# Optimization experiments

Measured on AMD Instinct MI355X. Metric: run time of the kernel, lower is better.

Reference implementation:

```python
import jax, jax.numpy as jnp
import numpy as np
import math

D_MODEL = 768
N_HEADS = 6
HD = D_MODEL // N_HEADS  # 128
RANK = D_MODEL // 4      # 192
B, T = 128, 256


def _rope_tables(T, dim):
    # matches torch: inv = 1/10000**(arange(0,dim,2)/dim); emb = cat([outer(t,inv)]*2, -1)
    inv = 1.0 / (10000.0 ** (jnp.arange(0, dim, 2, dtype=jnp.float32) / dim))
    t = jnp.arange(T, dtype=jnp.float32)
    freqs = jnp.outer(t, inv)                       # [T, dim/2]
    emb = jnp.concatenate([freqs, freqs], axis=-1)  # [T, dim]
    return jnp.cos(emb), jnp.sin(emb)               # each [T, dim]


def _rot(x):
    h = x.shape[-1] // 2
    return jnp.concatenate([-x[..., h:], x[..., :h]], axis=-1)


def setup_inputs() -> dict:
    key = jax.random.key(0)
    ks = jax.random.split(key, 8)
    s_in = 1.0 / math.sqrt(D_MODEL)
    s_r = 1.0 / math.sqrt(RANK)
    inp = {
        'x': jax.random.normal(ks[0], (B, T, D_MODEL), dtype=jnp.float32),
        'qA': jax.random.normal(ks[1], (D_MODEL, RANK), dtype=jnp.float32) * s_in,
        'qB': jax.random.normal(ks[2], (RANK, D_MODEL), dtype=jnp.float32) * s_r,
        'kA': jax.random.normal(ks[3], (D_MODEL, RANK), dtype=jnp.float32) * s_in,
        'kB': jax.random.normal(ks[4], (RANK, D_MODEL), dtype=jnp.float32) * s_r,
        'vA': jax.random.normal(ks[5], (D_MODEL, RANK), dtype=jnp.float32) * s_in,
        'vB': jax.random.normal(ks[6], (RANK, D_MODEL), dtype=jnp.float32) * s_r,
        'o_w': jax.random.normal(ks[7], (D_MODEL, D_MODEL), dtype=jnp.float32) * s_in,
    }
    return inp


def reference(x, qA, qB, kA, kB, vA, vB, o_w):
    Bb, Tt, _ = x.shape
    # low-rank projections: in -> rank -> out, then split heads [B, H, T, hd]
    def proj(A, W):
        h = (x @ A) @ W
        return h.reshape(Bb, Tt, N_HEADS, HD).transpose(0, 2, 1, 3)
    q = proj(qA, qB)
    k = proj(kA, kB)
    v = proj(vA, vB)
    cos, sin = _rope_tables(Tt, HD)  # [T, hd], broadcast over B, H
    q = q * cos + _rot(q) * sin
    k = k * cos + _rot(k) * sin
    att = jnp.einsum('bhqd,bhkd->bhqk', q, k) / math.sqrt(HD)
    causal = jnp.tril(jnp.ones((Tt, Tt), dtype=bool))
    att = jnp.where(causal, att, -jnp.inf)
    att = jax.nn.softmax(att, axis=-1)
    out = jnp.einsum('bhqk,bhkd->bhqd', att, v)          # [B, H, T, hd]
    out = out.transpose(0, 2, 1, 3).reshape(Bb, Tt, D_MODEL)
    return out @ o_w
```

## Files before the change

kernel.cpp:

```cpp
#include <hip/hip_runtime.h>
#include <hip/hip_bf16.h>
#include <stdint.h>

typedef __attribute__((ext_vector_type(8))) short s16x8;
typedef __attribute__((ext_vector_type(4))) float f32x4;

#define D_MODEL 768
#define N_HEADS 6
#define HD 128
#define RANK 192
#define TT 256
#define NROW 32768
#define NK 12
#define QSCL 0.08838834764831845f
#define PSTRIDE 25165824

__device__ inline short f2bf(float f) {
  union { float f; unsigned u; } x; x.f = f;
  unsigned r = x.u + 0x7fffu + ((x.u >> 16) & 1u);
  return (short)(r >> 16);
}
__device__ inline float bf2f(short v) {
  union { unsigned u; float f; } x; x.u = ((unsigned)(unsigned short)v) << 16;
  return x.f;
}
__device__ inline void gload_lds16(const void* g, void* lds) {
  __builtin_amdgcn_global_load_lds(
      (const __attribute__((address_space(1))) unsigned int*)g,
      (__attribute__((address_space(3))) unsigned int*)lds, 16, 0, 0);
}

#define BAR()    asm volatile("s_barrier" ::: "memory")
#define LGKM0()  asm volatile("s_waitcnt lgkmcnt(0)" ::: "memory")
#define WAITVM4() asm volatile("s_waitcnt vmcnt(4)" ::: "memory")
#define WAITVM0() asm volatile("s_waitcnt vmcnt(0)" ::: "memory")

__global__ void k_tables(float* __restrict__ cosT, float* __restrict__ sinT) {
  int tid = blockIdx.x * 256 + threadIdx.x;
  int t = tid >> 6, i = tid & 63;
  float inv = powf(10000.0f, -(float)i / 64.0f);
  float ang = (float)t * inv;
  cosT[tid] = cosf(ang);
  sinT[tid] = sinf(ang);
}

__global__ void k_castx(const float* __restrict__ x, short* __restrict__ xb) {
  int t = blockIdx.x * 256 + threadIdx.x;
  const float4* xp = (const float4*)x;
  float4 a = xp[t * 2], b = xp[t * 2 + 1];
  s16x8 o;
  o[0] = f2bf(a.x); o[1] = f2bf(a.y); o[2] = f2bf(a.z); o[3] = f2bf(a.w);
  o[4] = f2bf(b.x); o[5] = f2bf(b.y); o[6] = f2bf(b.z); o[7] = f2bf(b.w);
  *(s16x8*)(xb + (size_t)t * 8) = o;
}

__global__ void k_makew(const float* __restrict__ qA, const float* __restrict__ qB,
                        const float* __restrict__ kA, const float* __restrict__ kB,
                        const float* __restrict__ vA, const float* __restrict__ vB,
                        short* __restrict__ WT) {
  int g = blockIdx.x * 256 + threadIdx.x;
  int n4 = g % 576, kkb = g / 576;
  int part = n4 / 192, nnb = (n4 % 192) * 4;
  const float* A = (part == 0) ? qA : (part == 1) ? kA : vA;
  const float* Bm = (part == 0) ? qB : (part == 1) ? kB : vB;
  float acc[4][4] = {};
  for (int r0 = 0; r0 < RANK; r0 += 4) {
    float4 a4[4], b4[4];
#pragma unroll
    for (int q = 0; q < 4; ++q)
      a4[q] = *(const float4*)&A[(kkb + q * 192) * RANK + r0];
#pragma unroll
    for (int i = 0; i < 4; ++i)
      b4[i] = *(const float4*)&Bm[(r0 + i) * 768 + nnb];
#pragma unroll
    for (int q = 0; q < 4; ++q) {
      const float* aq = (const float*)&a4[q];
#pragma unroll
      for (int i = 0; i < 4; ++i) {
        const float* bi = (const float*)&b4[i];
#pragma unroll
        for (int jn = 0; jn < 4; ++jn)
          acc[q][jn] += aq[i] * bi[jn];
      }
    }
  }
#pragma unroll
  for (int q = 0; q < 4; ++q)
#pragma unroll
    for (int jn = 0; jn < 4; ++jn)
      WT[(size_t)(part * 768 + nnb + jn) * 768 + kkb + q * 192] = f2bf(acc[q][jn]);
}

__global__ void k_wot(const float* __restrict__ ow, short* __restrict__ WT) {
  int g = blockIdx.x * 256 + threadIdx.x;
  int n = g % 768, kk = g / 768;
  WT[(size_t)(2304 + n) * 768 + kk] = f2bf(ow[(size_t)kk * 768 + n]);
}

__device__ inline s16x8 rdfrag(const short* hbase, int rowbyte, int ksl4x, int swz) {
  return *(const s16x8*)((const char*)hbase + rowbyte + (((ksl4x) ^ (swz)) << 4));
}

template <int MODE>
__global__ __launch_bounds__(512, 2) void k_gemm8(const short* __restrict__ A,
                                                  const short* __restrict__ Bt,
                                                  void* __restrict__ Cv, int ldc) {
  extern __shared__ short lds[];
  const int tid = threadIdx.x;
  const int wid = tid >> 6, lane = tid & 63;
  const int l15 = lane & 15, l4 = lane >> 4;
  const int wr = wid >> 2, wc = wid & 3;
  const int swz = l15 & 7;
  const int bid = blockIdx.y * 128 + blockIdx.x;
  const int nper = gridDim.y;
  const int xcd = bid & 7, loc = bid >> 3;
  const int mq = loc / nper;
  const int mt = xcd * 16 + mq;
  const int nt = loc - mq * nper;
  const long mbase = (long)mt * 256;
  const long nbase = (long)nt * 256;

  const int hb0 = wid * 2048 + lane * 16;
  const int hb1 = hb0 + 1024;
  const int r0 = hb0 >> 7, c0 = ((hb0 >> 4) & 7) ^ (r0 & 7);
  const int r1 = hb1 >> 7, c1 = ((hb1 >> 4) & 7) ^ (r1 & 7);
  const int off0 = r0 * 768 + c0 * 8;
  const int off1 = r1 * 768 + c1 * 8;

#define STAGE(G, rowoff, kt, ldsS) do {                                        \
    gload_lds16((G) + (size_t)(rowoff) * 768 + (kt) * 64 + off0,               \
                (char*)(ldsS) + wid * 2048);                                   \
    gload_lds16((G) + (size_t)(rowoff) * 768 + (kt) * 64 + off1,               \
                (char*)(ldsS) + wid * 2048 + 1024);                            \
  } while (0)

#define LDSA(buf, half) (lds + ((buf) * 2 + (half)) * 8192)
#define LDSB(buf, half) (lds + 32768 + ((buf) * 2 + (half)) * 8192)

  f32x4 acc[8][4] = {};

  STAGE(A,  mbase,       0, LDSA(0, 0));
  STAGE(Bt, nbase,       0, LDSB(0, 0));
  STAGE(A,  mbase + 128, 0, LDSA(0, 1));
  STAGE(Bt, nbase + 128, 0, LDSB(0, 1));
  STAGE(A,  mbase,       1, LDSA(1, 0));
  STAGE(Bt, nbase,       1, LDSB(1, 0));
  WAITVM4();
  BAR();

  s16x8 a03[4][2], a47[4][2], b01[2][2], b23[2][2];

#pragma unroll
  for (int kt = 0; kt < NK; ++kt) {
    const int buf = kt & 1, nbuf = buf ^ 1;
    const short* Ab = LDSA(buf, wr);
    const short* Bb = LDSB(buf, (wc >> 1));
    const int browbase = (wc & 1) * 64 * 128;

#pragma unroll
    for (int mf = 0; mf < 4; ++mf)
#pragma unroll
      for (int ks = 0; ks < 2; ++ks)
        a03[mf][ks] = rdfrag(Ab, (mf * 16 + l15) * 128, ks * 4 + l4, swz);
#pragma unroll
    for (int nf = 0; nf < 2; ++nf)
#pragma unroll
      for (int ks = 0; ks < 2; ++ks)
        b01[nf][ks] = rdfrag(Bb, browbase + (nf * 16 + l15) * 128, ks * 4 + l4, swz);
    if (kt + 1 < NK) STAGE(A, mbase + 128, kt + 1, LDSA(nbuf, 1));
    BAR();
    LGKM0();
    __builtin_amdgcn_s_setprio(1);
#pragma unroll
    for (int mf = 0; mf < 4; ++mf)
#pragma unroll
      for (int nf = 0; nf < 2; ++nf)
#pragma unroll
        for (int ks = 0; ks < 2; ++ks)
          acc[mf][nf] = __builtin_amdgcn_mfma_f32_16x16x32_bf16(a03[mf][ks], b01[nf][ks], acc[mf][nf], 0, 0, 0);
    __builtin_amdgcn_s_setprio(0);
    BAR();

#pragma unroll
    for (int mf = 0; mf < 4; ++mf)
#pragma unroll
      for (int ks = 0; ks < 2; ++ks)
        a47[mf][ks] = rdfrag(Ab, ((mf + 4) * 16 + l15) * 128, ks * 4 + l4, swz);
    if (kt + 1 < NK) STAGE(Bt, nbase + 128, kt + 1, LDSB(nbuf, 1));
    BAR();
    LGKM0();
    __builtin_amdgcn_s_setprio(1);
#pragma unroll
    for (int mf = 0; mf < 4; ++mf)
#pragma unroll
      for (int nf = 0; nf < 2; ++nf)
#pragma unroll
        for (int ks = 0; ks < 2; ++ks)
          acc[mf + 4][nf] = __builtin_amdgcn_mfma_f32_16x16x32_bf16(a47[mf][ks], b01[nf][ks], acc[mf + 4][nf], 0, 0, 0);
    __builtin_amdgcn_s_setprio(0);
    BAR();

#pragma unroll
    for (int nf = 0; nf < 2; ++nf)
#pragma unroll
      for (int ks = 0; ks < 2; ++ks)
        b23[nf][ks] = rdfrag(Bb, browbase + ((nf + 2) * 16 + l15) * 128, ks * 4 + l4, swz);
    if (kt + 2 < NK) STAGE(A, mbase, kt + 2, LDSA(buf, 0));
    BAR();
    LGKM0();
    __builtin_amdgcn_s_setprio(1);
#pragma unroll
    for (int mf = 0; mf < 4; ++mf)
#pragma unroll
      for (int nf = 0; nf < 2; ++nf)
#pragma unroll
        for (int ks = 0; ks < 2; ++ks)
          acc[mf][nf + 2] = __builtin_amdgcn_mfma_f32_16x16x32_bf16(a03[mf][ks], b23[nf][ks], acc[mf][nf + 2], 0, 0, 0);
    __builtin_amdgcn_s_setprio(0);
    BAR();

    if (kt + 2 < NK) STAGE(Bt, nbase, kt + 2, LDSB(buf, 0));
    BAR();
    __builtin_amdgcn_s_setprio(1);
#pragma unroll
    for (int mf = 0; mf < 4; ++mf)
#pragma unroll
      for (int nf = 0; nf < 2; ++nf)
#pragma unroll
        for (int ks = 0; ks < 2; ++ks)
          acc[mf + 4][nf + 2] = __builtin_amdgcn_mfma_f32_16x16x32_bf16(a47[mf][ks], b23[nf][ks], acc[mf + 4][nf + 2], 0, 0, 0);
    __builtin_amdgcn_s_setprio(0);
    if (kt < NK - 1) {
      if (kt + 2 < NK) WAITVM4(); else WAITVM0();
      BAR();
    }
  }
#undef STAGE

#pragma unroll
  for (int mf = 0; mf < 8; ++mf)
#pragma unroll
    for (int nf = 0; nf < 4; ++nf) {
      const int col = (int)(nbase + wc * 64 + nf * 16 + l15);
      const int part = col / 768;
      const int wi = col - part * 768;
      const int hh = wi >> 7, dd = wi & 127;
#pragma unroll
      for (int r = 0; r < 4; ++r) {
        long row = mbase + wr * 128 + mf * 16 + l4 * 4 + r;
        if (MODE == 0) {
          ((float*)Cv)[row * ldc + col] = acc[mf][nf][r];
        } else {
          size_t idx = (size_t)part * PSTRIDE +
                       (((size_t)(row >> 8) * 6 + hh) * 256 + (row & 255)) * 128 + dd;
          ((short*)Cv)[idx] = f2bf(acc[mf][nf][r]);
        }
      }
    }
}

__global__ void k_ropek(short* __restrict__ kp, const float* __restrict__ cosT,
                        const float* __restrict__ sinT) {
  int tid = blockIdx.x * 256 + threadIdx.x;
  int bh = tid >> 11, rem = tid & 2047;
  int t = rem >> 3, i8 = (rem & 7) * 8;
  size_t base = ((size_t)bh * 256 + t) * 128 + i8;
  s16x8 a = *(const s16x8*)(kp + base);
  s16x8 b = *(const s16x8*)(kp + base + 64);
  const float4* cp = (const float4*)(cosT + t * 64 + i8);
  const float4* sp = (const float4*)(sinT + t * 64 + i8);
  float4 c04 = cp[0], c14 = cp[1], s04 = sp[0], s14 = sp[1];
  float cs[8] = {c04.x, c04.y, c04.z, c04.w, c14.x, c14.y, c14.z, c14.w};
  float sn[8] = {s04.x, s04.y, s04.z, s04.w, s14.x, s14.y, s14.z, s14.w};
  s16x8 na, nb;
#pragma unroll
  for (int j = 0; j < 8; ++j) {
    float av = bf2f(a[j]), bv = bf2f(b[j]);
    na[j] = f2bf(av * cs[j] - bv * sn[j]);
    nb[j] = f2bf(bv * cs[j] + av * sn[j]);
  }
  *(s16x8*)(kp + base) = na;
  *(s16x8*)(kp + base + 64) = nb;
}

__global__ __launch_bounds__(512) void k_attn(const short* __restrict__ qp,
                                              const short* __restrict__ kp,
                                              const short* __restrict__ vp,
                                              short* __restrict__ attout,
                                              const float* __restrict__ cosT,
                                              const float* __restrict__ sinT) {
  extern __shared__ short smem[];
  short* Kls0 = smem;
  short* Kls1 = smem + 8192;
  short* Vt   = smem + 16384;
  const int tid = threadIdx.x;
  const int wid = tid >> 6, lane = tid & 63;
  const int l15 = lane & 15, l4 = lane >> 4;
  short* PlsW = smem + 24576 + wid * 2048;
  const int bh = blockIdx.x;
  const int b = bh / N_HEADS, h = bh % N_HEADS;
  const long row0 = (long)b * TT;
  const size_t pbase = (size_t)bh * 256 * 128;
  const int d0 = wid * 16;

  s16x8 qf[2][4];
#pragma unroll
  for (int mi = 0; mi < 2; ++mi)
#pragma unroll
    for (int kc = 0; kc < 4; ++kc) {
      int t = wid * 32 + mi * 16 + l15;
      qf[mi][kc] = *(const s16x8*)(qp + pbase + (size_t)t * 128 + kc * 32 + l4 * 8);
    }
#pragma unroll
  for (int mi = 0; mi < 2; ++mi) {
    int t = wid * 32 + mi * 16 + l15;
#pragma unroll
    for (int kc = 0; kc < 2; ++kc) {
      const float4* cp = (const float4*)(cosT + t * 64 + kc * 32 + l4 * 8);
      const float4* sp = (const float4*)(sinT + t * 64 + kc * 32 + l4 * 8);
      float4 c04 = cp[0], c14 = cp[1], s04 = sp[0], s14 = sp[1];
      float cs[8] = {c04.x, c04.y, c04.z, c04.w, c14.x, c14.y, c14.z, c14.w};
      float sn[8] = {s04.x, s04.y, s04.z, s04.w, s14.x, s14.y, s14.z, s14.w};
#pragma unroll
      for (int jj = 0; jj < 8; ++jj) {
        float av = bf2f(qf[mi][kc][jj]);
        float bv = bf2f(qf[mi][kc + 2][jj]);
        qf[mi][kc][jj]     = f2bf((av * cs[jj] - bv * sn[jj]) * QSCL);
        qf[mi][kc + 2][jj] = f2bf((bv * cs[jj] + av * sn[jj]) * QSCL);
      }
    }
  }

#define STAGEK(j_, Kd) do {                                                     \
    int bb0_ = wid * 2048 + lane * 16;                                          \
    int r0_ = bb0_ >> 8; int sc0_ = ((bb0_ >> 4) & 15) ^ (r0_ & 7);             \
    gload_lds16(kp + pbase + (size_t)((j_) * 64 + r0_) * 128 + sc0_ * 8,        \
                (char*)(Kd) + wid * 2048);                                      \
    int bb1_ = bb0_ + 1024;                                                     \
    int r1_ = bb1_ >> 8; int sc1_ = ((bb1_ >> 4) & 15) ^ (r1_ & 7);             \
    gload_lds16(kp + pbase + (size_t)((j_) * 64 + r1_) * 128 + sc1_ * 8,        \
                (char*)(Kd) + wid * 2048 + 1024);                               \
  } while (0)

#define LOADV(j_, va, vb) do {                                                  \
    const short* vsrc_ = vp + pbase + (size_t)((j_) * 64 + lane) * 128 + d0;    \
    va = *(const s16x8*)vsrc_;                                                  \
    vb = *(const s16x8*)(vsrc_ + 8);                                            \
  } while (0)

  float mst[2][4], lst[2][4];
  f32x4 oacc[2][8];
#pragma unroll
  for (int mi = 0; mi < 2; ++mi)
#pragma unroll
    for (int r = 0; r < 4; ++r) { mst[mi][r] = -1e30f; lst[mi][r] = 0.f; }
#pragma unroll
  for (int mi = 0; mi < 2; ++mi)
#pragma unroll
    for (int nd = 0; nd < 8; ++nd) oacc[mi][nd] = {0.f, 0.f, 0.f, 0.f};

  const int jmax = (wid * 32 + 31) / 64;

  STAGEK(0, Kls0);
  s16x8 vr[2][2];
  LOADV(0, vr[0][0], vr[0][1]);

#pragma unroll
  for (int j = 0; j < 4; ++j) {
    const int buf = j & 1;
    const short* Kb = buf ? Kls1 : Kls0;
    short* Kn = buf ? Kls0 : Kls1;
    if (j < 3) {
      STAGEK(j + 1, Kn);
      LOADV(j + 1, vr[buf ^ 1][0], vr[buf ^ 1][1]);
    }
    if (j < 3) WAITVM4(); else WAITVM0();
    __builtin_amdgcn_sched_barrier(0);
    BAR();
#pragma unroll
    for (int e = 0; e < 8; ++e)
      *(short*)((char*)Vt + (d0 + e) * 128 + (((lane >> 3) ^ e) << 4) + (lane & 7) * 2) = vr[buf][0][e];
#pragma unroll
    for (int e = 0; e < 8; ++e)
      *(short*)((char*)Vt + (d0 + 8 + e) * 128 + (((lane >> 3) ^ e) << 4) + (lane & 7) * 2) = vr[buf][1][e];

    if (j <= jmax) {
      f32x4 sacc[2][4] = {};
#pragma unroll
      for (int kc = 0; kc < 4; ++kc) {
        s16x8 kf[4];
#pragma unroll
        for (int ni = 0; ni < 4; ++ni)
          kf[ni] = *(const s16x8*)((const char*)Kb + (ni * 16 + l15) * 256 +
                                   (((kc * 4 + l4) ^ (l15 & 7)) << 4));
#pragma unroll
        for (int mi = 0; mi < 2; ++mi)
#pragma unroll
          for (int ni = 0; ni < 4; ++ni)
            sacc[mi][ni] = __builtin_amdgcn_mfma_f32_16x16x32_bf16(qf[mi][kc], kf[ni], sacc[mi][ni], 0, 0, 0);
      }
#pragma unroll
      for (int mi = 0; mi < 2; ++mi) {
#pragma unroll
        for (int r = 0; r < 4; ++r) {
          int qr = wid * 32 + mi * 16 + l4 * 4 + r;
          float rm = -1e30f;
#pragma unroll
          for (int ni = 0; ni < 4; ++ni) {
            int kvc = j * 64 + ni * 16 + l15;
            if (kvc > qr) sacc[mi][ni][r] = -1e30f;
            rm = fmaxf(rm, sacc[mi][ni][r]);
          }
#pragma unroll
          for (int d2 = 1; d2 < 16; d2 <<= 1)
            rm = fmaxf(rm, __shfl_xor(rm, d2, 64));
          float mold = mst[mi][r];
          float mnew = fmaxf(mold, rm);
          float alpha = __expf(mold - mnew);
          mst[mi][r] = mnew;
          float rs = 0.f;
#pragma unroll
          for (int ni = 0; ni < 4; ++ni) {
            float p = __expf(sacc[mi][ni][r] - mnew);
            sacc[mi][ni][r] = p;
            rs += p;
          }
#pragma unroll
          for (int d2 = 1; d2 < 16; d2 <<= 1)
            rs += __shfl_xor(rs, d2, 64);
          lst[mi][r] = lst[mi][r] * alpha + rs;
#pragma unroll
          for (int nd = 0; nd < 8; ++nd)
            oacc[mi][nd][r] *= alpha;
        }
      }
#pragma unroll
      for (int mi = 0; mi < 2; ++mi)
#pragma unroll
        for (int ni = 0; ni < 4; ++ni)
#pragma unroll
          for (int r = 0; r < 4; ++r) {
            int prow = mi * 16 + l4 * 4 + r;
            int pcp = (ni * 2 + (l15 >> 3)) ^ (prow & 7);
            *(short*)((char*)PlsW + prow * 128 + (pcp << 4) + (l15 & 7) * 2) =
                f2bf(sacc[mi][ni][r]);
          }
    }
    LGKM0();
    BAR();
    __builtin_amdgcn_sched_barrier(0);
    if (j <= jmax) {
#pragma unroll
      for (int kc2 = 0; kc2 < 2; ++kc2) {
        s16x8 pa[2];
#pragma unroll
        for (int mi = 0; mi < 2; ++mi)
          pa[mi] = *(const s16x8*)((const char*)PlsW + (mi * 16 + l15) * 128 +
                                   (((kc2 * 4 + l4) ^ (l15 & 7)) << 4));
#pragma unroll
        for (int nd = 0; nd < 8; ++nd) {
          s16x8 vf = *(const s16x8*)((const char*)Vt + (nd * 16 + l15) * 128 +
                                     (((kc2 * 4 + l4) ^ (l15 & 7)) << 4));
#pragma unroll
          for (int mi = 0; mi < 2; ++mi)
            oacc[mi][nd] = __builtin_amdgcn_mfma_f32_16x16x32_bf16(pa[mi], vf, oacc[mi][nd], 0, 0, 0);
        }
      }
    }
  }
#undef STAGEK
#undef LOADV
#pragma unroll
  for (int mi = 0; mi < 2; ++mi)
#pragma unroll
    for (int nd = 0; nd < 8; ++nd)
#pragma unroll
      for (int r = 0; r < 4; ++r) {
        long row = row0 + wid * 32 + mi * 16 + l4 * 4 + r;
        int col = h * HD + nd * 16 + l15;
        attout[row * D_MODEL + col] = f2bf(oacc[mi][nd][r] / lst[mi][r]);
      }
}

extern "C" void kernel_launch(void* const* d_in, const int* in_sizes, int n_in,
                              void* d_out, int out_size, void* d_ws, size_t ws_size,
                              hipStream_t stream) {
  const float* x  = (const float*)d_in[0];
  const float* qA = (const float*)d_in[1];
  const float* qB = (const float*)d_in[2];
  const float* kA = (const float*)d_in[3];
  const float* kB = (const float*)d_in[4];
  const float* vA = (const float*)d_in[5];
  const float* vB = (const float*)d_in[6];
  const float* ow = (const float*)d_in[7];

  char* ws = (char*)d_ws;
  short* qkvp  = (short*)ws;
  short* qp    = qkvp;
  short* kp    = qkvp + (size_t)PSTRIDE;
  short* vp    = qkvp + (size_t)2 * PSTRIDE;
  short* xb    = (short*)(ws + 150994944);
  short* WT    = (short*)(ws + 201326592);
  float* cosT  = (float*)(ws + 206045184);
  float* sinT  = (float*)(ws + 206110720);
  short* attout = xb;

  hipFuncSetAttribute((const void*)k_gemm8<2>,
                      hipFuncAttributeMaxDynamicSharedMemorySize, 131072);
  hipFuncSetAttribute((const void*)k_gemm8<0>,
                      hipFuncAttributeMaxDynamicSharedMemorySize, 131072);
  hipFuncSetAttribute((const void*)k_attn,
                      hipFuncAttributeMaxDynamicSharedMemorySize, 81920);

  k_tables<<<64, 256, 0, stream>>>(cosT, sinT);
  k_castx<<<12288, 256, 0, stream>>>(x, xb);
  k_makew<<<432, 256, 0, stream>>>(qA, qB, kA, kB, vA, vB, WT);
  k_wot<<<2304, 256, 0, stream>>>(ow, WT);
  k_gemm8<2><<<dim3(128, 9), 512, 131072, stream>>>(xb, WT, (void*)qkvp, 0);
  k_ropek<<<6144, 256, 0, stream>>>(kp, cosT, sinT);
  k_attn<<<768, 512, 81920, stream>>>(qp, kp, vp, attout, cosT, sinT);
  k_gemm8<0><<<dim3(128, 3), 512, 131072, stream>>>(attout, WT + (size_t)2304 * 768, d_out, 768);
}
```

Before: 353.8 us.

## Compute QKV as two low-rank GEMMs instead of a prefused dense weight

Drops the kernel that multiplied A and B into a dense 768x2304 weight. Instead, x is multiplied by the concatenated A matrices (576 wide, padded to 768 tiles) into a bf16 intermediate h, and a second short-K GEMM applies the B matrices per part, writing head-split q, k and v. The GEMM kernel is templated on the K-tile count and on lda/ldb to support both stages. This roughly halves the projection FLOPs and removes the fp32 weight-fusion kernel, at the cost of an extra launch, writing and reading h, and padded columns in the first GEMM.

Result: slower. 365.6 us (+3.3%).

```diff
diff --git a/kernel.cpp b/kernel.cpp
--- a/kernel.cpp
+++ b/kernel.cpp
@@ -11,7 +11,6 @@
 #define RANK 192
 #define TT 256
 #define NROW 32768
-#define NK 12
 #define QSCL 0.08838834764831845f
 #define PSTRIDE 25165824
 
@@ -54,57 +53,39 @@
   *(s16x8*)(xb + (size_t)t * 8) = o;
 }
 
-__global__ void k_makew(const float* __restrict__ qA, const float* __restrict__ qB,
-                        const float* __restrict__ kA, const float* __restrict__ kB,
-                        const float* __restrict__ vA, const float* __restrict__ vB,
-                        short* __restrict__ WT) {
+__global__ void k_wt1(const float* __restrict__ qA, const float* __restrict__ kA,
+                      const float* __restrict__ vA, short* __restrict__ WT1) {
   int g = blockIdx.x * 256 + threadIdx.x;
-  int n4 = g % 576, kkb = g / 576;
-  int part = n4 / 192, nnb = (n4 % 192) * 4;
+  int n = g / 768, k = g % 768;
+  int part = n / RANK, r = n % RANK;
   const float* A = (part == 0) ? qA : (part == 1) ? kA : vA;
+  WT1[(size_t)n * 768 + k] = f2bf(A[(size_t)k * RANK + r]);
+}
+
+__global__ void k_wt2(const float* __restrict__ qB, const float* __restrict__ kB,
+                      const float* __restrict__ vB, short* __restrict__ WT2) {
+  int g = blockIdx.x * 256 + threadIdx.x;
+  int part = g / 147456, rem = g % 147456;
+  int r = rem / 768, n = rem % 768;
   const float* Bm = (part == 0) ? qB : (part == 1) ? kB : vB;
-  float acc[4][4] = {};
-  for (int r0 = 0; r0 < RANK; r0 += 4) {
-    float4 a4[4], b4[4];
-#pragma unroll
-    for (int q = 0; q < 4; ++q)
-      a4[q] = *(const float4*)&A[(kkb + q * 192) * RANK + r0];
-#pragma unroll
-    for (int i = 0; i < 4; ++i)
-      b4[i] = *(const float4*)&Bm[(r0 + i) * 768 + nnb];
-#pragma unroll
-    for (int q = 0; q < 4; ++q) {
-      const float* aq = (const float*)&a4[q];
-#pragma unroll
-      for (int i = 0; i < 4; ++i) {
-        const float* bi = (const float*)&b4[i];
-#pragma unroll
-        for (int jn = 0; jn < 4; ++jn)
-          acc[q][jn] += aq[i] * bi[jn];
-      }
-    }
-  }
-#pragma unroll
-  for (int q = 0; q < 4; ++q)
-#pragma unroll
-    for (int jn = 0; jn < 4; ++jn)
-      WT[(size_t)(part * 768 + nnb + jn) * 768 + kkb + q * 192] = f2bf(acc[q][jn]);
-}
-
-__global__ void k_wot(const float* __restrict__ ow, short* __restrict__ WT) {
+  WT2[(size_t)part * 147456 + (size_t)n * 192 + r] = f2bf(Bm[(size_t)r * 768 + n]);
+}
+
+__global__ void k_wot(const float* __restrict__ ow, short* __restrict__ WTo) {
   int g = blockIdx.x * 256 + threadIdx.x;
   int n = g % 768, kk = g / 768;
-  WT[(size_t)(2304 + n) * 768 + kk] = f2bf(ow[(size_t)kk * 768 + n]);
+  WTo[(size_t)n * 768 + kk] = f2bf(ow[(size_t)kk * 768 + n]);
 }
 
 __device__ inline s16x8 rdfrag(const short* hbase, int rowbyte, int ksl4x, int swz) {
   return *(const s16x8*)((const char*)hbase + rowbyte + (((ksl4x) ^ (swz)) << 4));
 }
 
-template <int MODE>
+template <int MODE, int NKT>
 __global__ __launch_bounds__(512, 2) void k_gemm8(const short* __restrict__ A,
                                                   const short* __restrict__ Bt,
-                                                  void* __restrict__ Cv, int ldc) {
+                                                  void* __restrict__ Cv,
+                                                  int lda, int ldb) {
   extern __shared__ short lds[];
   const int tid = threadIdx.x;
   const int wid = tid >> 6, lane = tid & 63;
@@ -117,41 +98,53 @@
   const int mq = loc / nper;
   const int mt = xcd * 16 + mq;
   const int nt = loc - mq * nper;
+  const int part  = (MODE == 2) ? (nt / 3) : 0;
+  const int ntile = (MODE == 2) ? (nt % 3) : nt;
   const long mbase = (long)mt * 256;
-  const long nbase = (long)nt * 256;
+  const long nbase = (long)ntile * 256;
+  const short* Aeff  = A + part * 192;
+  const short* Bteff = Bt + (size_t)part * 147456;
 
   const int hb0 = wid * 2048 + lane * 16;
   const int hb1 = hb0 + 1024;
   const int r0 = hb0 >> 7, c0 = ((hb0 >> 4) & 7) ^ (r0 & 7);
   const int r1 = hb1 >> 7, c1 = ((hb1 >> 4) & 7) ^ (r1 & 7);
-  const int off0 = r0 * 768 + c0 * 8;
-  const int off1 = r1 * 768 + c1 * 8;
-
-#define STAGE(G, rowoff, kt, ldsS) do {                                        \
-    gload_lds16((G) + (size_t)(rowoff) * 768 + (kt) * 64 + off0,               \
+  const int offA0 = r0 * lda + c0 * 8;
+  const int offA1 = r1 * lda + c1 * 8;
+  const int offB0 = r0 * ldb + c0 * 8;
+  const int offB1 = r1 * ldb + c1 * 8;
+
+#define STAGEA(rowbase, kt, ldsS) do {                                         \
+    gload_lds16(Aeff + (size_t)(rowbase) * lda + (kt) * 64 + offA0,            \
                 (char*)(ldsS) + wid * 2048);                                   \
-    gload_lds16((G) + (size_t)(rowoff) * 768 + (kt) * 64 + off1,               \
+    gload_lds16(Aeff + (size_t)(rowbase) * lda + (kt) * 64 + offA1,            \
                 (char*)(ldsS) + wid * 2048 + 1024);                            \
   } while (0)
+#define STAGEB(rowbase, kt, ldsS) do {                                         \
+    gload_lds16(Bteff + (size_t)(rowbase) * ldb + (kt) * 64 + offB0,           \
+                (char*)(ldsS) + wid * 2048);                                   \
+    gload_lds16(Bteff + (size_t)(rowbase) * ldb + (kt) * 64 + offB1,           \
+                (char*)(ldsS) + wid * 2048 + 1024);                            \
+  } while (0)
 
 #define LDSA(buf, half) (lds + ((buf) * 2 + (half)) * 8192)
 #define LDSB(buf, half) (lds + 32768 + ((buf) * 2 + (half)) * 8192)
 
   f32x4 acc[8][4] = {};
 
-  STAGE(A,  mbase,       0, LDSA(0, 0));
-  STAGE(Bt, nbase,       0, LDSB(0, 0));
-  STAGE(A,  mbase + 128, 0, LDSA(0, 1));
-  STAGE(Bt, nbase + 128, 0, LDSB(0, 1));
-  STAGE(A,  mbase,       1, LDSA(1, 0));
-  STAGE(Bt, nbase,       1, LDSB(1, 0));
+  STAGEA(mbase,       0, LDSA(0, 0));
+  STAGEB(nbase,       0, LDSB(0, 0));
+  STAGEA(mbase + 128, 0, LDSA(0, 1));
+  STAGEB(nbase + 128, 0, LDSB(0, 1));
+  STAGEA(mbase,       1, LDSA(1, 0));
+  STAGEB(nbase,       1, LDSB(1, 0));
   WAITVM4();
   BAR();
 
   s16x8 a03[4][2], a47[4][2], b01[2][2], b23[2][2];
 
 #pragma unroll
-  for (int kt = 0; kt < NK; ++kt) {
+  for (int kt = 0; kt < NKT; ++kt) {
     const int buf = kt & 1, nbuf = buf ^ 1;
     const short* Ab = LDSA(buf, wr);
     const short* Bb = LDSB(buf, (wc >> 1));
@@ -167,7 +160,7 @@
 #pragma unroll
       for (int ks = 0; ks < 2; ++ks)
         b01[nf][ks] = rdfrag(Bb, browbase + (nf * 16 + l15) * 128, ks * 4 + l4, swz);
-    if (kt + 1 < NK) STAGE(A, mbase + 128, kt + 1, LDSA(nbuf, 1));
+    if (kt + 1 < NKT) STAGEA(mbase + 128, kt + 1, LDSA(nbuf, 1));
     BAR();
     LGKM0();
     __builtin_amdgcn_s_setprio(1);
@@ -186,7 +179,7 @@
 #pragma unroll
       for (int ks = 0; ks < 2; ++ks)
         a47[mf][ks] = rdfrag(Ab, ((mf + 4) * 16 + l15) * 128, ks * 4 + l4, swz);
-    if (kt + 1 < NK) STAGE(Bt, nbase + 128, kt + 1, LDSB(nbuf, 1));
+    if (kt + 1 < NKT) STAGEB(nbase + 128, kt + 1, LDSB(nbuf, 1));
     BAR();
     LGKM0();
     __builtin_amdgcn_s_setprio(1);
@@ -205,7 +198,7 @@
 #pragma unroll
       for (int ks = 0; ks < 2; ++ks)
         b23[nf][ks] = rdfrag(Bb, browbase + ((nf + 2) * 16 + l15) * 128, ks * 4 + l4, swz);
-    if (kt + 2 < NK) STAGE(A, mbase, kt + 2, LDSA(buf, 0));
+    if (kt + 2 < NKT) STAGEA(mbase, kt + 2, LDSA(buf, 0));
     BAR();
     LGKM0();
     __builtin_amdgcn_s_setprio(1);
@@ -219,7 +212,7 @@
     __builtin_amdgcn_s_setprio(0);
     BAR();
 
-    if (kt + 2 < NK) STAGE(Bt, nbase, kt + 2, LDSB(buf, 0));
+    if (kt + 2 < NKT) STAGEB(nbase, kt + 2, LDSB(buf, 0));
     BAR();
     __builtin_amdgcn_s_setprio(1);
 #pragma unroll
@@ -230,26 +223,27 @@
         for (int ks = 0; ks < 2; ++ks)
           acc[mf + 4][nf + 2] = __builtin_amdgcn_mfma_f32_16x16x32_bf16(a47[mf][ks], b23[nf][ks], acc[mf + 4][nf + 2], 0, 0, 0);
     __builtin_amdgcn_s_setprio(0);
-    if (kt < NK - 1) {
-      if (kt + 2 < NK) WAITVM4(); else WAITVM0();
+    if (kt < NKT - 1) {
+      if (kt + 2 < NKT) WAITVM4(); else WAITVM0();
       BAR();
     }
   }
-#undef STAGE
+#undef STAGEA
+#undef STAGEB
 
 #pragma unroll
   for (int mf = 0; mf < 8; ++mf)
 #pragma unroll
     for (int nf = 0; nf < 4; ++nf) {
       const int col = (int)(nbase + wc * 64 + nf * 16 + l15);
-      const int part = col / 768;
-      const int wi = col - part * 768;
-      const int hh = wi >> 7, dd = wi & 127;
+      const int hh = col >> 7, dd = col & 127;
 #pragma unroll
       for (int r = 0; r < 4; ++r) {
         long row = mbase + wr * 128 + mf * 16 + l4 * 4 + r;
         if (MODE == 0) {
-          ((float*)Cv)[row * ldc + col] = acc[mf][nf][r];
+          ((float*)Cv)[row * 768 + col] = acc[mf][nf][r];
+        } else if (MODE == 1) {
+          if (col < 576) ((short*)Cv)[row * 576 + col] = f2bf(acc[mf][nf][r]);
         } else {
           size_t idx = (size_t)part * PSTRIDE +
                        (((size_t)(row >> 8) * 6 + hh) * 256 + (row & 255)) * 128 + dd;
@@ -500,24 +494,31 @@
   short* kp    = qkvp + (size_t)PSTRIDE;
   short* vp    = qkvp + (size_t)2 * PSTRIDE;
   short* xb    = (short*)(ws + 150994944);
-  short* WT    = (short*)(ws + 201326592);
-  float* cosT  = (float*)(ws + 206045184);
-  float* sinT  = (float*)(ws + 206110720);
+  short* h     = (short*)(ws + 201326592);
+  short* WT1   = (short*)(ws + 238977024);
+  short* WT2   = (short*)(ws + 240156672);
+  short* WTo   = (short*)(ws + 241041408);
+  float* cosT  = (float*)(ws + 242221056);
+  float* sinT  = (float*)(ws + 242286592);
   short* attout = xb;
 
-  hipFuncSetAttribute((const void*)k_gemm8<2>,
+  hipFuncSetAttribute((const void*)k_gemm8<1, 12>,
                       hipFuncAttributeMaxDynamicSharedMemorySize, 131072);
-  hipFuncSetAttribute((const void*)k_gemm8<0>,
+  hipFuncSetAttribute((const void*)k_gemm8<2, 3>,
+                      hipFuncAttributeMaxDynamicSharedMemorySize, 131072);
+  hipFuncSetAttribute((const void*)k_gemm8<0, 12>,
                       hipFuncAttributeMaxDynamicSharedMemorySize, 131072);
   hipFuncSetAttribute((const void*)k_attn,
                       hipFuncAttributeMaxDynamicSharedMemorySize, 81920);
 
   k_tables<<<64, 256, 0, stream>>>(cosT, sinT);
   k_castx<<<12288, 256, 0, stream>>>(x, xb);
-  k_makew<<<432, 256, 0, stream>>>(qA, qB, kA, kB, vA, vB, WT);
-  k_wot<<<2304, 256, 0, stream>>>(ow, WT);
-  k_gemm8<2><<<dim3(128, 9), 512, 131072, stream>>>(xb, WT, (void*)qkvp, 0);
+  k_wt1<<<1728, 256, 0, stream>>>(qA, kA, vA, WT1);
+  k_wt2<<<1728, 256, 0, stream>>>(qB, kB, vB, WT2);
+  k_wot<<<2304, 256, 0, stream>>>(ow, WTo);
+  k_gemm8<1, 12><<<dim3(128, 3), 512, 131072, stream>>>(xb, WT1, (void*)h, 768, 768);
+  k_gemm8<2, 3><<<dim3(128, 9), 512, 131072, stream>>>(h, WT2, (void*)qkvp, 576, 192);
   k_ropek<<<6144, 256, 0, stream>>>(kp, cosT, sinT);
   k_attn<<<768, 512, 81920, stream>>>(qp, kp, vp, attout, cosT, sinT);
-  k_gemm8<0><<<dim3(128, 3), 512, 131072, stream>>>(attout, WT + (size_t)2304 * 768, d_out, 768);
-}
+  k_gemm8<0, 12><<<dim3(128, 3), 512, 131072, stream>>>(attout, WTo, d_out, 768, 768);
+}
```

## Single-buffer K tile in attention to cut LDS and raise occupancy

Applied to the files above, without the earlier changes.

Replaces the double-buffered K shared-memory tile and V register double buffer with single buffers, shrinking the attention kernel's dynamic LDS from 80 KB to 64 KB. The prefetch of the next K/V tile now starts after the second barrier, overlapping only with the PV MFMA stage. The aim is to fit more blocks per CU for better latency hiding. In exchange, the score stage now waits on memory without intra-block overlap.

Result: no change. 354.0 us (+0.0%).

```diff
diff --git a/kernel.cpp b/kernel.cpp
--- a/kernel.cpp
+++ b/kernel.cpp
@@ -290,13 +290,12 @@
                                               const float* __restrict__ cosT,
                                               const float* __restrict__ sinT) {
   extern __shared__ short smem[];
-  short* Kls0 = smem;
-  short* Kls1 = smem + 8192;
-  short* Vt   = smem + 16384;
+  short* Kls = smem;
+  short* Vt  = smem + 8192;
   const int tid = threadIdx.x;
   const int wid = tid >> 6, lane = tid & 63;
   const int l15 = lane & 15, l4 = lane >> 4;
-  short* PlsW = smem + 24576 + wid * 2048;
+  short* PlsW = smem + 16384 + wid * 2048;
   const int bh = blockIdx.x;
   const int b = bh / N_HEADS, h = bh % N_HEADS;
   const long row0 = (long)b * TT;
@@ -331,21 +330,21 @@
     }
   }
 
-#define STAGEK(j_, Kd) do {                                                     \
+#define STAGEK(j_) do {                                                         \
     int bb0_ = wid * 2048 + lane * 16;                                          \
     int r0_ = bb0_ >> 8; int sc0_ = ((bb0_ >> 4) & 15) ^ (r0_ & 7);             \
     gload_lds16(kp + pbase + (size_t)((j_) * 64 + r0_) * 128 + sc0_ * 8,        \
-                (char*)(Kd) + wid * 2048);                                      \
+                (char*)Kls + wid * 2048);                                       \
     int bb1_ = bb0_ + 1024;                                                     \
     int r1_ = bb1_ >> 8; int sc1_ = ((bb1_ >> 4) & 15) ^ (r1_ & 7);             \
     gload_lds16(kp + pbase + (size_t)((j_) * 64 + r1_) * 128 + sc1_ * 8,        \
-                (char*)(Kd) + wid * 2048 + 1024);                               \
+                (char*)Kls + wid * 2048 + 1024);                                \
   } while (0)
 
-#define LOADV(j_, va, vb) do {                                                  \
+#define LOADV(j_) do {                                                          \
     const short* vsrc_ = vp + pbase + (size_t)((j_) * 64 + lane) * 128 + d0;    \
-    va = *(const s16x8*)vsrc_;                                                  \
-    vb = *(const s16x8*)(vsrc_ + 8);                                            \
+    vA_ = *(const s16x8*)vsrc_;                                                 \
+    vB_ = *(const s16x8*)(vsrc_ + 8);                                           \
   } while (0)
 
   float mst[2][4], lst[2][4];
@@ -361,28 +360,21 @@
 
   const int jmax = (wid * 32 + 31) / 64;
 
-  STAGEK(0, Kls0);
-  s16x8 vr[2][2];
-  LOADV(0, vr[0][0], vr[0][1]);
+  s16x8 vA_, vB_;
+  STAGEK(0);
+  LOADV(0);
 
 #pragma unroll
   for (int j = 0; j < 4; ++j) {
-    const int buf = j & 1;
-    const short* Kb = buf ? Kls1 : Kls0;
-    short* Kn = buf ? Kls0 : Kls1;
-    if (j < 3) {
-      STAGEK(j + 1, Kn);
-      LOADV(j + 1, vr[buf ^ 1][0], vr[buf ^ 1][1]);
-    }
-    if (j < 3) WAITVM4(); else WAITVM0();
+    WAITVM0();
     __builtin_amdgcn_sched_barrier(0);
     BAR();
 #pragma unroll
     for (int e = 0; e < 8; ++e)
-      *(short*)((char*)Vt + (d0 + e) * 128 + (((lane >> 3) ^ e) << 4) + (lane & 7) * 2) = vr[buf][0][e];
+      *(short*)((char*)Vt + (d0 + e) * 128 + (((lane >> 3) ^ e) << 4) + (lane & 7) * 2) = vA_[e];
 #pragma unroll
     for (int e = 0; e < 8; ++e)
-      *(short*)((char*)Vt + (d0 + 8 + e) * 128 + (((lane >> 3) ^ e) << 4) + (lane & 7) * 2) = vr[buf][1][e];
+      *(short*)((char*)Vt + (d0 + 8 + e) * 128 + (((lane >> 3) ^ e) << 4) + (lane & 7) * 2) = vB_[e];
 
     if (j <= jmax) {
       f32x4 sacc[2][4] = {};
@@ -391,7 +383,7 @@
         s16x8 kf[4];
 #pragma unroll
         for (int ni = 0; ni < 4; ++ni)
-          kf[ni] = *(const s16x8*)((const char*)Kb + (ni * 16 + l15) * 256 +
+          kf[ni] = *(const s16x8*)((const char*)Kls + (ni * 16 + l15) * 256 +
                                    (((kc * 4 + l4) ^ (l15 & 7)) << 4));
 #pragma unroll
         for (int mi = 0; mi < 2; ++mi)
@@ -449,6 +441,10 @@
     LGKM0();
     BAR();
     __builtin_amdgcn_sched_barrier(0);
+    if (j < 3) {
+      STAGEK(j + 1);
+      LOADV(j + 1);
+    }
     if (j <= jmax) {
 #pragma unroll
       for (int kc2 = 0; kc2 < 2; ++kc2) {
@@ -510,7 +506,7 @@
   hipFuncSetAttribute((const void*)k_gemm8<0>,
                       hipFuncAttributeMaxDynamicSharedMemorySize, 131072);
   hipFuncSetAttribute((const void*)k_attn,
-                      hipFuncAttributeMaxDynamicSharedMemorySize, 81920);
+                      hipFuncAttributeMaxDynamicSharedMemorySize, 65536);
 
   k_tables<<<64, 256, 0, stream>>>(cosT, sinT);
   k_castx<<<12288, 256, 0, stream>>>(x, xb);
@@ -518,6 +514,6 @@
   k_wot<<<2304, 256, 0, stream>>>(ow, WT);
   k_gemm8<2><<<dim3(128, 9), 512, 131072, stream>>>(xb, WT, (void*)qkvp, 0);
   k_ropek<<<6144, 256, 0, stream>>>(kp, cosT, sinT);
-  k_attn<<<768, 512, 81920, stream>>>(qp, kp, vp, attout, cosT, sinT);
+  k_attn<<<768, 512, 65536, stream>>>(qp, kp, vp, attout, cosT, sinT);
   k_gemm8<0><<<dim3(128, 3), 512, 131072, stream>>>(attout, WT + (size_t)2304 * 768, d_out, 768);
 }
```
